# Kernel tuning notes

Hardware: AMD Instinct MI355X
Metric: run time of the kernel (lower is better)

The kernel has to match this reference:

```python
import jax, jax.numpy as jnp
import numpy as np

B, S, D_IN, H, D_HEAD = 4, 2048, 768, 12, 64


def setup_inputs() -> dict:
    key = jax.random.key(0)
    kx, kq, kk, kv, kc = jax.random.split(key, 5)
    x = jax.random.normal(kx, (B, S, D_IN), dtype=jnp.float32)
    # torch.rand -> uniform [0,1)
    wq = jax.random.uniform(kq, (H, D_IN, D_HEAD), dtype=jnp.float32)
    wk = jax.random.uniform(kk, (H, D_IN, D_HEAD), dtype=jnp.float32)
    wv = jax.random.uniform(kv, (H, D_IN, D_HEAD), dtype=jnp.float32)
    wc = jax.random.uniform(kc, (D_HEAD, H * D_HEAD), dtype=jnp.float32)
    return {"x": x, "wq": wq, "wk": wk, "wv": wv, "wc": wc}


def reference(x, wq, wk, wv, wc):
    # per-head projections: weight [H, D_in, D_head], x [B, S, D_in] -> [B, H, S, D_head]
    q = jnp.einsum('hkd,bsk->bhsd', wq, x)
    k = jnp.einsum('hkd,bsk->bhsd', wk, x)
    v = jnp.einsum('hkd,bsk->bhsd', wv, x)
    scale = jnp.sqrt(jnp.float32(D_HEAD))
    scores = jax.nn.softmax(jnp.einsum('bhld,bhnd->bhln', q, k) / scale, axis=-1)
    z = jnp.einsum('bhln,bhnd->bhld', scores, v)        # [B, H, S, D_head]
    z = jnp.transpose(z, (0, 2, 1, 3)).reshape(B, S, H * D_HEAD)
    # output projection: wc [D_head, H*D_head] -> [B, S, D_head]
    return jnp.einsum('ij,bsj->bsi', wc, z)
```

## Files before the change

### kernel.cpp

```cpp
#include <hip/hip_runtime.h>
#include <hip/hip_bf16.h>
#include <math.h>

#define BB 4
#define SS 2048
#define DIN 768
#define HH 12
#define DH 64
#define NT (SS / 64)

typedef __attribute__((ext_vector_type(8))) _Float16 f16x8;
typedef __attribute__((ext_vector_type(4))) _Float16 f16x4;
typedef __attribute__((ext_vector_type(2))) _Float16 f16x2;
typedef __attribute__((ext_vector_type(4))) float f32x4;
typedef __attribute__((ext_vector_type(16))) float f32x16;
typedef __attribute__((ext_vector_type(4))) unsigned u32x4;

__device__ inline void splith(float v, _Float16& hi, _Float16& lo) {
    hi = (_Float16)v;
    lo = (_Float16)(v - (float)hi);
}
__device__ inline unsigned packh2(float a, float b) {
    f16x2 h; h[0] = (_Float16)a; h[1] = (_Float16)b;
    return __builtin_bit_cast(unsigned, h);
}
__device__ inline f16x8 ldb64x2(const _Float16* p) {
    const uint2* q = reinterpret_cast<const uint2*>(p);
    uint2 a = q[0], b = q[1];
    u32x4 u = {a.x, a.y, b.x, b.y};
    return __builtin_bit_cast(f16x8, u);
}
__device__ inline void stb64x2(_Float16* p, uint4 v) {
    uint2* q = reinterpret_cast<uint2*>(p);
    q[0] = make_uint2(v.x, v.y);
    q[1] = make_uint2(v.z, v.w);
}
__device__ inline f32x16 zero16() {
    f32x16 v;
    #pragma unroll
    for (int i = 0; i < 16; ++i) v[i] = 0.f;
    return v;
}

__global__ __launch_bounds__(256) void prep_kernel(
    const float* __restrict__ x,
    const float* __restrict__ wq, const float* __restrict__ wk, const float* __restrict__ wv,
    const float* __restrict__ wc,
    _Float16* __restrict__ whi, _Float16* __restrict__ wlo,
    _Float16* __restrict__ wch, _Float16* __restrict__ wcl,
    _Float16* __restrict__ xh, _Float16* __restrict__ xl)
{
    __shared__ float tile[64][65];
    const int bid = blockIdx.x;
    const int t = threadIdx.x;

    if (bid < 432) {
        const int kt = bid % 12, h = (bid / 12) % 12, which = bid / 144;
        const float* w = (which == 0) ? wq : (which == 1) ? wk : wv;
        w += (size_t)h * (DIN * DH);
        const size_t plane = ((size_t)which * HH + h) * (size_t)(64 * DIN);
        {
            int r = t >> 2, n0 = (t & 3) * 16;
            const float* src = w + (size_t)(kt * 64 + r) * DH + n0;
            #pragma unroll
            for (int q = 0; q < 4; ++q) {
                float4 v = *reinterpret_cast<const float4*>(src + q * 4);
                tile[r][n0 + q * 4 + 0] = v.x; tile[r][n0 + q * 4 + 1] = v.y;
                tile[r][n0 + q * 4 + 2] = v.z; tile[r][n0 + q * 4 + 3] = v.w;
            }
        }
        __syncthreads();
        {
            int n = t >> 2, k0 = (t & 3) * 16;
            f16x8 h0, h1, l0, l1;
            #pragma unroll
            for (int j = 0; j < 8; ++j) {
                _Float16 hh, ll;
                splith(tile[k0 + j][n], hh, ll);     h0[j] = hh; l0[j] = ll;
                splith(tile[k0 + 8 + j][n], hh, ll); h1[j] = hh; l1[j] = ll;
            }
            size_t base = plane + (size_t)n * DIN + kt * 64 + k0;
            *reinterpret_cast<f16x8*>(whi + base)     = h0;
            *reinterpret_cast<f16x8*>(whi + base + 8) = h1;
            *reinterpret_cast<f16x8*>(wlo + base)     = l0;
            *reinterpret_cast<f16x8*>(wlo + base + 8) = l1;
        }
    } else if (bid < 456) {
        int idx = ((bid - 432) * 256 + t) * 8;
        float4 a = *reinterpret_cast<const float4*>(wc + idx);
        float4 b = *reinterpret_cast<const float4*>(wc + idx + 4);
        float f[8] = {a.x, a.y, a.z, a.w, b.x, b.y, b.z, b.w};
        f16x8 hv, lv;
        #pragma unroll
        for (int j = 0; j < 8; ++j) {
            _Float16 hh, ll;
            splith(f[j], hh, ll);
            hv[j] = hh; lv[j] = ll;
        }
        *reinterpret_cast<f16x8*>(wch + idx) = hv;
        *reinterpret_cast<f16x8*>(wcl + idx) = lv;
    } else {
        int idx = ((bid - 456) * 256 + t) * 8;
        float4 a = *reinterpret_cast<const float4*>(x + idx);
        float4 b = *reinterpret_cast<const float4*>(x + idx + 4);
        float f[8] = {a.x, a.y, a.z, a.w, b.x, b.y, b.z, b.w};
        f16x8 hv, lv;
        #pragma unroll
        for (int j = 0; j < 8; ++j) {
            _Float16 hh, ll;
            splith(f[j], hh, ll);
            hv[j] = hh; lv[j] = ll;
        }
        *reinterpret_cast<f16x8*>(xh + idx) = hv;
        *reinterpret_cast<f16x8*>(xl + idx) = lv;
    }
}

__global__ __launch_bounds__(256) void qkv_proj_kernel(
    const _Float16* __restrict__ xh, const _Float16* __restrict__ xl,
    const _Float16* __restrict__ whi, const _Float16* __restrict__ wlo,
    _Float16* __restrict__ qh, _Float16* __restrict__ ql,
    _Float16* __restrict__ kh, _Float16* __restrict__ kl,
    _Float16* __restrict__ vt)
{
    const int flat = blockIdx.x;
    const int xcd  = flat & 7;
    const int rest = flat >> 3;
    const int mt   = xcd * 8 + (rest & 7);
    const int hw   = rest >> 3;
    const int which = hw / HH, h = hw % HH;
    const int m0 = mt * 128;
    const size_t wplane = ((size_t)which * HH + h) * (size_t)(64 * DIN);

    __shared__ _Float16 xbuf[10240];
    __shared__ _Float16 wsh[64][40], wsl[64][40];

    const int t = threadIdx.x;
    const int lane = t & 63, wid = t >> 6;
    const int fr = lane & 15, fg = lane >> 4, g8 = fg * 8;

    f32x4 acc[2][4];
    #pragma unroll
    for (int g = 0; g < 2; ++g)
        #pragma unroll
        for (int n = 0; n < 4; ++n) acc[g][n] = (f32x4){0.f, 0.f, 0.f, 0.f};

    for (int ks = 0; ks < DIN / 32; ++ks) {
        const int k0 = ks * 32;
        __syncthreads();
        {
            int r = t >> 1, cb = (t & 1) * 16;
            const size_t xb = (size_t)(m0 + r) * DIN + k0 + cb;
            *reinterpret_cast<uint4*>(&xbuf[r * 40 + cb])            = *reinterpret_cast<const uint4*>(xh + xb);
            *reinterpret_cast<uint4*>(&xbuf[r * 40 + cb + 8])        = *reinterpret_cast<const uint4*>(xh + xb + 8);
            *reinterpret_cast<uint4*>(&xbuf[5120 + r * 40 + cb])     = *reinterpret_cast<const uint4*>(xl + xb);
            *reinterpret_cast<uint4*>(&xbuf[5120 + r * 40 + cb + 8]) = *reinterpret_cast<const uint4*>(xl + xb + 8);
            int rw = t >> 2, c8 = (t & 3) * 8;
            size_t wb = wplane + (size_t)rw * DIN + k0 + c8;
            *reinterpret_cast<uint4*>(&wsh[rw][c8]) = *reinterpret_cast<const uint4*>(whi + wb);
            *reinterpret_cast<uint4*>(&wsl[rw][c8]) = *reinterpret_cast<const uint4*>(wlo + wb);
        }
        __syncthreads();

        f16x8 ah0 = *reinterpret_cast<const f16x8*>(&xbuf[(wid * 32 + fr) * 40 + g8]);
        f16x8 al0 = *reinterpret_cast<const f16x8*>(&xbuf[5120 + (wid * 32 + fr) * 40 + g8]);
        f16x8 ah1 = *reinterpret_cast<const f16x8*>(&xbuf[(wid * 32 + 16 + fr) * 40 + g8]);
        f16x8 al1 = *reinterpret_cast<const f16x8*>(&xbuf[5120 + (wid * 32 + 16 + fr) * 40 + g8]);
        #pragma unroll
        for (int n = 0; n < 4; ++n) {
            f16x8 bh = *reinterpret_cast<const f16x8*>(&wsh[n * 16 + fr][g8]);
            f16x8 bl = *reinterpret_cast<const f16x8*>(&wsl[n * 16 + fr][g8]);
            acc[0][n] = __builtin_amdgcn_mfma_f32_16x16x32_f16(ah0, bh, acc[0][n], 0, 0, 0);
            acc[0][n] = __builtin_amdgcn_mfma_f32_16x16x32_f16(ah0, bl, acc[0][n], 0, 0, 0);
            acc[0][n] = __builtin_amdgcn_mfma_f32_16x16x32_f16(al0, bh, acc[0][n], 0, 0, 0);
            acc[1][n] = __builtin_amdgcn_mfma_f32_16x16x32_f16(ah1, bh, acc[1][n], 0, 0, 0);
            acc[1][n] = __builtin_amdgcn_mfma_f32_16x16x32_f16(ah1, bl, acc[1][n], 0, 0, 0);
            acc[1][n] = __builtin_amdgcn_mfma_f32_16x16x32_f16(al1, bh, acc[1][n], 0, 0, 0);
        }
    }

    const int b0 = m0 >> 11, s0 = m0 & 2047;
    if (which == 2) {
        __syncthreads();
        #pragma unroll
        for (int g = 0; g < 2; ++g)
            #pragma unroll
            for (int n = 0; n < 4; ++n)
                #pragma unroll
                for (int j = 0; j < 4; ++j)
                    xbuf[(n * 16 + fr) * 136 + wid * 32 + g * 16 + fg * 4 + j] =
                        (_Float16)acc[g][n][j];
        __syncthreads();
        int rr = t >> 2, c0 = (t & 3) * 32;
        size_t base = (((size_t)b0 * HH + h) * DH + rr) * SS + s0 + c0;
        #pragma unroll
        for (int q = 0; q < 4; ++q)
            *reinterpret_cast<uint4*>(vt + base + q * 8) =
                *reinterpret_cast<uint4*>(&xbuf[rr * 136 + c0 + q * 8]);
    } else {
        #pragma unroll
        for (int g = 0; g < 2; ++g)
            #pragma unroll
            for (int n = 0; n < 4; ++n)
                #pragma unroll
                for (int j = 0; j < 4; ++j) {
                    int row = wid * 32 + g * 16 + fg * 4 + j;
                    size_t idx = (((size_t)b0 * HH + h) * SS + s0 + row) * DH + n * 16 + fr;
                    float val = acc[g][n][j];
                    if (which == 0) val *= 0.125f;
                    _Float16 hi, lo;
                    splith(val, hi, lo);
                    if (which == 0) { qh[idx] = hi; ql[idx] = lo; }
                    else            { kh[idx] = hi; kl[idx] = lo; }
                }
    }
}

__global__ __launch_bounds__(256, 3) void attn_kernel(
    const _Float16* __restrict__ qhp, const _Float16* __restrict__ qlp,
    const _Float16* __restrict__ khp, const _Float16* __restrict__ klp,
    const _Float16* __restrict__ vtp,
    _Float16* __restrict__ z)
{
    const int flat = blockIdx.x;
    const int remap = (flat & 7) * 96 + (flat >> 3);
    const int qt = remap & 15;
    const int h  = (remap >> 4) % HH;
    const int b  = remap / (16 * HH);

    const size_t headbase = ((size_t)b * HH + h) * (size_t)(SS * DH);
    const _Float16* Qh = qhp + headbase;
    const _Float16* Ql = qlp + headbase;
    const _Float16* Kh = khp + headbase;
    const _Float16* Kl = klp + headbase;
    const _Float16* Vt = vtp + headbase;

    __shared__ _Float16 ksh[64][68], ksl[64][68], vts[64][68];

    const int t = threadIdx.x;
    const int lane = t & 63, w = t >> 6;
    const int qcol = lane & 31, hi = lane >> 5;
    const int r4 = t >> 2, c16 = (t & 3) * 16;

    const size_t qbase = (size_t)(qt * 128 + w * 32 + qcol) * DH + hi * 8;
    f16x8 bqh[4], bql[4];
    #pragma unroll
    for (int ks = 0; ks < 4; ++ks) {
        bqh[ks] = *reinterpret_cast<const f16x8*>(Qh + qbase + 16 * ks);
        bql[ks] = *reinterpret_cast<const f16x8*>(Ql + qbase + 16 * ks);
    }

    uint4 rk0, rk1, rl0, rl1, rv0, rv1;
    auto prefetch = [&](int kt) {
        size_t sk = (size_t)(kt * 64 + r4) * DH + c16;
        rk0 = *reinterpret_cast<const uint4*>(Kh + sk);
        rk1 = *reinterpret_cast<const uint4*>(Kh + sk + 8);
        rl0 = *reinterpret_cast<const uint4*>(Kl + sk);
        rl1 = *reinterpret_cast<const uint4*>(Kl + sk + 8);
        size_t sv = (size_t)r4 * SS + kt * 64 + c16;
        rv0 = *reinterpret_cast<const uint4*>(Vt + sv);
        rv1 = *reinterpret_cast<const uint4*>(Vt + sv + 8);
    };
    prefetch(0);

    float mrun = -INFINITY, lrun = 0.f;
    f32x16 oc0 = zero16(), oc1 = zero16();

    for (int kt = 0; kt < NT; ++kt) {
        __syncthreads();
        stb64x2(&ksh[r4][c16],     rk0);
        stb64x2(&ksh[r4][c16 + 8], rk1);
        stb64x2(&ksl[r4][c16],     rl0);
        stb64x2(&ksl[r4][c16 + 8], rl1);
        stb64x2(&vts[r4][c16],     rv0);
        stb64x2(&vts[r4][c16 + 8], rv1);
        if (kt + 1 < NT) prefetch(kt + 1);
        __syncthreads();

        f32x16 c0 = zero16(), c1 = zero16();
        #pragma unroll
        for (int ks = 0; ks < 4; ++ks) {
            const int doff = hi * 8 + 16 * ks;
            f16x8 a0h = ldb64x2(&ksh[qcol][doff]);
            f16x8 a0l = ldb64x2(&ksl[qcol][doff]);
            c0 = __builtin_amdgcn_mfma_f32_32x32x16_f16(a0h, bqh[ks], c0, 0, 0, 0);
            c0 = __builtin_amdgcn_mfma_f32_32x32x16_f16(a0h, bql[ks], c0, 0, 0, 0);
            c0 = __builtin_amdgcn_mfma_f32_32x32x16_f16(a0l, bqh[ks], c0, 0, 0, 0);
            f16x8 a1h = ldb64x2(&ksh[qcol + 32][doff]);
            f16x8 a1l = ldb64x2(&ksl[qcol + 32][doff]);
            c1 = __builtin_amdgcn_mfma_f32_32x32x16_f16(a1h, bqh[ks], c1, 0, 0, 0);
            c1 = __builtin_amdgcn_mfma_f32_32x32x16_f16(a1h, bql[ks], c1, 0, 0, 0);
            c1 = __builtin_amdgcn_mfma_f32_32x32x16_f16(a1l, bqh[ks], c1, 0, 0, 0);
        }

        float mx = c0[0];
        #pragma unroll
        for (int i = 1; i < 16; ++i) mx = fmaxf(mx, c0[i]);
        #pragma unroll
        for (int i = 0; i < 16; ++i) mx = fmaxf(mx, c1[i]);
        mx = fmaxf(mx, __shfl_xor(mx, 32));
        float nm = fmaxf(mrun, mx);
        float corr = __expf(mrun - nm);
        float sum = 0.f;
        #pragma unroll
        for (int i = 0; i < 16; ++i) { float p = __expf(c0[i] - nm); c0[i] = p; sum += p; }
        #pragma unroll
        for (int i = 0; i < 16; ++i) { float p = __expf(c1[i] - nm); c1[i] = p; sum += p; }
        sum += __shfl_xor(sum, 32);
        lrun = lrun * corr + sum;
        mrun = nm;
        #pragma unroll
        for (int i = 0; i < 16; ++i) { oc0[i] *= corr; oc1[i] *= corr; }

        auto mk = [](float s0, float s1, float s2, float s3,
                     float s4, float s5, float s6, float s7) -> f16x8 {
            unsigned a0 = packh2(s0, s1), a1 = packh2(s2, s3);
            unsigned b0 = packh2(s4, s5), b1 = packh2(s6, s7);
            asm volatile("v_permlane32_swap_b32 %0, %1" : "+v"(a0), "+v"(b0));
            asm volatile("v_permlane32_swap_b32 %0, %1" : "+v"(a1), "+v"(b1));
            u32x4 u = {a0, a1, b0, b1};
            return __builtin_bit_cast(f16x8, u);
        };
        f16x8 bp0 = mk(c0[0], c0[1], c0[2],  c0[3],  c0[4],  c0[5],  c0[6],  c0[7]);
        f16x8 bp1 = mk(c0[8], c0[9], c0[10], c0[11], c0[12], c0[13], c0[14], c0[15]);
        f16x8 bp2 = mk(c1[0], c1[1], c1[2],  c1[3],  c1[4],  c1[5],  c1[6],  c1[7]);
        f16x8 bp3 = mk(c1[8], c1[9], c1[10], c1[11], c1[12], c1[13], c1[14], c1[15]);

        {
            const int k0 = hi * 8;
            f16x8 av;
            av = ldb64x2(&vts[qcol][k0]);            oc0 = __builtin_amdgcn_mfma_f32_32x32x16_f16(av, bp0, oc0, 0, 0, 0);
            av = ldb64x2(&vts[qcol + 32][k0]);       oc1 = __builtin_amdgcn_mfma_f32_32x32x16_f16(av, bp0, oc1, 0, 0, 0);
            av = ldb64x2(&vts[qcol][k0 + 16]);       oc0 = __builtin_amdgcn_mfma_f32_32x32x16_f16(av, bp1, oc0, 0, 0, 0);
            av = ldb64x2(&vts[qcol + 32][k0 + 16]);  oc1 = __builtin_amdgcn_mfma_f32_32x32x16_f16(av, bp1, oc1, 0, 0, 0);
            av = ldb64x2(&vts[qcol][k0 + 32]);       oc0 = __builtin_amdgcn_mfma_f32_32x32x16_f16(av, bp2, oc0, 0, 0, 0);
            av = ldb64x2(&vts[qcol + 32][k0 + 32]);  oc1 = __builtin_amdgcn_mfma_f32_32x32x16_f16(av, bp2, oc1, 0, 0, 0);
            av = ldb64x2(&vts[qcol][k0 + 48]);       oc0 = __builtin_amdgcn_mfma_f32_32x32x16_f16(av, bp3, oc0, 0, 0, 0);
            av = ldb64x2(&vts[qcol + 32][k0 + 48]);  oc1 = __builtin_amdgcn_mfma_f32_32x32x16_f16(av, bp3, oc1, 0, 0, 0);
        }
    }

    float inv = 1.0f / lrun;
    size_t zb = ((size_t)b * SS + qt * 128 + w * 32 + qcol) * (size_t)(HH * DH) + h * DH;
    #pragma unroll
    for (int g = 0; g < 4; ++g) {
        f16x4 v0, v1;
        #pragma unroll
        for (int i = 0; i < 4; ++i) {
            v0[i] = (_Float16)(oc0[4 * g + i] * inv);
            v1[i] = (_Float16)(oc1[4 * g + i] * inv);
        }
        *reinterpret_cast<f16x4*>(z + zb + 8 * g + 4 * hi)      = v0;
        *reinterpret_cast<f16x4*>(z + zb + 32 + 8 * g + 4 * hi) = v1;
    }
}

__global__ __launch_bounds__(256) void outproj_kernel(
    const _Float16* __restrict__ z,
    const _Float16* __restrict__ wch, const _Float16* __restrict__ wcl,
    float* __restrict__ out)
{
    const int mt = blockIdx.x, m0 = mt * 64;
    __shared__ _Float16 zs[64][40], wh_[64][40], wl_[64][40];

    const int t = threadIdx.x;
    const int lane = t & 63, wid = t >> 6;
    const int fr = lane & 15, fg = lane >> 4, g8 = fg * 8;

    f32x4 acc[4];
    #pragma unroll
    for (int n = 0; n < 4; ++n) acc[n] = (f32x4){0.f, 0.f, 0.f, 0.f};

    for (int ks = 0; ks < DIN / 32; ++ks) {
        const int k0 = ks * 32;
        {
            int r = t >> 2, c8 = (t & 3) * 8;
            *reinterpret_cast<f16x8*>(&zs[r][c8]) =
                *reinterpret_cast<const f16x8*>(z + (size_t)(m0 + r) * DIN + k0 + c8);
            size_t wb = (size_t)r * DIN + k0 + c8;
            *reinterpret_cast<f16x8*>(&wh_[r][c8]) = *reinterpret_cast<const f16x8*>(wch + wb);
            *reinterpret_cast<f16x8*>(&wl_[r][c8]) = *reinterpret_cast<const f16x8*>(wcl + wb);
        }
        __syncthreads();
        f16x8 az = *reinterpret_cast<const f16x8*>(&zs[wid * 16 + fr][g8]);
        #pragma unroll
        for (int n = 0; n < 4; ++n) {
            f16x8 bh = *reinterpret_cast<const f16x8*>(&wh_[n * 16 + fr][g8]);
            f16x8 bl = *reinterpret_cast<const f16x8*>(&wl_[n * 16 + fr][g8]);
            acc[n] = __builtin_amdgcn_mfma_f32_16x16x32_f16(az, bh, acc[n], 0, 0, 0);
            acc[n] = __builtin_amdgcn_mfma_f32_16x16x32_f16(az, bl, acc[n], 0, 0, 0);
        }
        __syncthreads();
    }

    #pragma unroll
    for (int n = 0; n < 4; ++n)
        #pragma unroll
        for (int j = 0; j < 4; ++j) {
            int row = m0 + wid * 16 + fg * 4 + j;
            out[(size_t)row * DH + n * 16 + fr] = acc[n][j];
        }
}

extern "C" void kernel_launch(void* const* d_in, const int* in_sizes, int n_in,
                              void* d_out, int out_size, void* d_ws, size_t ws_size,
                              hipStream_t stream) {
    const float* x  = (const float*)d_in[0];
    const float* wq = (const float*)d_in[1];
    const float* wk = (const float*)d_in[2];
    const float* wv = (const float*)d_in[3];
    const float* wc = (const float*)d_in[4];
    float* out = (float*)d_out;

    const size_t wpl   = (size_t)3 * HH * 64 * DIN;
    const size_t plane = (size_t)BB * HH * SS * DH;
    _Float16* whi = (_Float16*)d_ws;
    _Float16* wlo = whi + wpl;
    _Float16* wch = wlo + wpl;
    _Float16* wcl = wch + (size_t)64 * DIN;
    _Float16* qh  = wcl + (size_t)64 * DIN;
    _Float16* ql  = qh + plane;
    _Float16* kh  = ql + plane;
    _Float16* kl  = kh + plane;
    _Float16* vt  = kl + plane;
    _Float16* xh  = vt + plane;
    _Float16* xl  = xh + plane;
    _Float16* zz  = xh;

    prep_kernel<<<3528, 256, 0, stream>>>(x, wq, wk, wv, wc, whi, wlo, wch, wcl, xh, xl);
    qkv_proj_kernel<<<2304, 256, 0, stream>>>(xh, xl, whi, wlo, qh, ql, kh, kl, vt);
    attn_kernel<<<768, 256, 0, stream>>>(qh, ql, kh, kl, vt, zz);
    outproj_kernel<<<128, 256, 0, stream>>>(zz, wch, wcl, out);
}
```

Measured before the change: 243.9 us.

## Load X fragments directly to registers and prefetch next k-step in QKV projection

The QKV projection no longer stages the activation tile through shared memory. Each wave loads its A fragments straight from global memory into registers, and the loads for the next k-step are issued before the compute of the current one, giving software pipelining with register double-buffering. Only the weight tile still goes through LDS, and a dedicated vtile buffer is used for the V transpose. A launch-bounds occupancy hint is also added. This trades redundant uncoalesced-ish global reads and higher register use for less LDS traffic and latency hiding.

```diff
diff --git a/kernel.cpp b/kernel.cpp
--- a/kernel.cpp
+++ b/kernel.cpp
@@ -116,7 +116,7 @@
     }
 }
 
-__global__ __launch_bounds__(256) void qkv_proj_kernel(
+__global__ __launch_bounds__(256, 3) void qkv_proj_kernel(
     const _Float16* __restrict__ xh, const _Float16* __restrict__ xl,
     const _Float16* __restrict__ whi, const _Float16* __restrict__ wlo,
     _Float16* __restrict__ qh, _Float16* __restrict__ ql,
@@ -132,12 +132,16 @@
     const int m0 = mt * 128;
     const size_t wplane = ((size_t)which * HH + h) * (size_t)(64 * DIN);
 
-    __shared__ _Float16 xbuf[10240];
     __shared__ _Float16 wsh[64][40], wsl[64][40];
+    __shared__ _Float16 vtile[64][136];
 
     const int t = threadIdx.x;
     const int lane = t & 63, wid = t >> 6;
     const int fr = lane & 15, fg = lane >> 4, g8 = fg * 8;
+    const int rw = t >> 2, c8 = (t & 3) * 8;
+
+    const size_t xr0 = (size_t)(m0 + wid * 32 + fr) * DIN;
+    const size_t xr1 = xr0 + (size_t)16 * DIN;
 
     f32x4 acc[2][4];
     #pragma unroll
@@ -145,27 +149,30 @@
         #pragma unroll
         for (int n = 0; n < 4; ++n) acc[g][n] = (f32x4){0.f, 0.f, 0.f, 0.f};
 
+    uint4 pah0, pal0, pah1, pal1, pwh, pwl;
+    auto pre = [&](int ks) {
+        const int off = ks * 32 + g8;
+        pah0 = *reinterpret_cast<const uint4*>(xh + xr0 + off);
+        pal0 = *reinterpret_cast<const uint4*>(xl + xr0 + off);
+        pah1 = *reinterpret_cast<const uint4*>(xh + xr1 + off);
+        pal1 = *reinterpret_cast<const uint4*>(xl + xr1 + off);
+        const size_t wb = wplane + (size_t)rw * DIN + ks * 32 + c8;
+        pwh = *reinterpret_cast<const uint4*>(whi + wb);
+        pwl = *reinterpret_cast<const uint4*>(wlo + wb);
+    };
+    pre(0);
+
     for (int ks = 0; ks < DIN / 32; ++ks) {
-        const int k0 = ks * 32;
-        __syncthreads();
-        {
-            int r = t >> 1, cb = (t & 1) * 16;
-            const size_t xb = (size_t)(m0 + r) * DIN + k0 + cb;
-            *reinterpret_cast<uint4*>(&xbuf[r * 40 + cb])            = *reinterpret_cast<const uint4*>(xh + xb);
-            *reinterpret_cast<uint4*>(&xbuf[r * 40 + cb + 8])        = *reinterpret_cast<const uint4*>(xh + xb + 8);
-            *reinterpret_cast<uint4*>(&xbuf[5120 + r * 40 + cb])     = *reinterpret_cast<const uint4*>(xl + xb);
-            *reinterpret_cast<uint4*>(&xbuf[5120 + r * 40 + cb + 8]) = *reinterpret_cast<const uint4*>(xl + xb + 8);
-            int rw = t >> 2, c8 = (t & 3) * 8;
-            size_t wb = wplane + (size_t)rw * DIN + k0 + c8;
-            *reinterpret_cast<uint4*>(&wsh[rw][c8]) = *reinterpret_cast<const uint4*>(whi + wb);
-            *reinterpret_cast<uint4*>(&wsl[rw][c8]) = *reinterpret_cast<const uint4*>(wlo + wb);
-        }
-        __syncthreads();
-
-        f16x8 ah0 = *reinterpret_cast<const f16x8*>(&xbuf[(wid * 32 + fr) * 40 + g8]);
-        f16x8 al0 = *reinterpret_cast<const f16x8*>(&xbuf[5120 + (wid * 32 + fr) * 40 + g8]);
-        f16x8 ah1 = *reinterpret_cast<const f16x8*>(&xbuf[(wid * 32 + 16 + fr) * 40 + g8]);
-        f16x8 al1 = *reinterpret_cast<const f16x8*>(&xbuf[5120 + (wid * 32 + 16 + fr) * 40 + g8]);
+        __syncthreads();
+        *reinterpret_cast<uint4*>(&wsh[rw][c8]) = pwh;
+        *reinterpret_cast<uint4*>(&wsl[rw][c8]) = pwl;
+        f16x8 ah0 = __builtin_bit_cast(f16x8, pah0);
+        f16x8 al0 = __builtin_bit_cast(f16x8, pal0);
+        f16x8 ah1 = __builtin_bit_cast(f16x8, pah1);
+        f16x8 al1 = __builtin_bit_cast(f16x8, pal1);
+        if (ks + 1 < DIN / 32) pre(ks + 1);
+        __syncthreads();
+
         #pragma unroll
         for (int n = 0; n < 4; ++n) {
             f16x8 bh = *reinterpret_cast<const f16x8*>(&wsh[n * 16 + fr][g8]);
@@ -181,22 +188,20 @@
 
     const int b0 = m0 >> 11, s0 = m0 & 2047;
     if (which == 2) {
-        __syncthreads();
         #pragma unroll
         for (int g = 0; g < 2; ++g)
             #pragma unroll
             for (int n = 0; n < 4; ++n)
                 #pragma unroll
                 for (int j = 0; j < 4; ++j)
-                    xbuf[(n * 16 + fr) * 136 + wid * 32 + g * 16 + fg * 4 + j] =
-                        (_Float16)acc[g][n][j];
+                    vtile[n * 16 + fr][wid * 32 + g * 16 + fg * 4 + j] = (_Float16)acc[g][n][j];
         __syncthreads();
         int rr = t >> 2, c0 = (t & 3) * 32;
         size_t base = (((size_t)b0 * HH + h) * DH + rr) * SS + s0 + c0;
         #pragma unroll
         for (int q = 0; q < 4; ++q)
             *reinterpret_cast<uint4*>(vt + base + q * 8) =
-                *reinterpret_cast<uint4*>(&xbuf[rr * 136 + c0 + q * 8]);
+                *reinterpret_cast<uint4*>(&vtile[rr][c0 + q * 8]);
     } else {
         #pragma unroll
         for (int g = 0; g < 2; ++g)
```

Measured after the change: 251.7 us. +3.2%, slower.
